# Performance work log

Hardware: AMD Instinct MI355X
Metric: run time of the kernel (lower is better)

## Reference

```python
import jax, jax.numpy as jnp
import numpy as np

N_HEADS = 12
NEG_BIG = 1e10  # matches torch source's -10000000000.0 masking constant


def setup_inputs() -> dict:
    key = jax.random.key(0)
    ks = jax.random.split(key, 5)
    nb, ns, nf = 4, 2048, 768
    return {
        "x": jax.random.normal(ks[0], (nb, ns, nf), dtype=jnp.float32),
        "Wqkv_w": jax.random.normal(ks[1], (3 * nf, nf), dtype=jnp.float32) * 0.02,
        "Wqkv_b": jax.random.normal(ks[2], (3 * nf,), dtype=jnp.float32) * 0.02,
        "Wproj_w": jax.random.normal(ks[3], (nf, nf), dtype=jnp.float32) * 0.02,
        "Wproj_b": jax.random.normal(ks[4], (nf,), dtype=jnp.float32) * 0.02,
    }


def reference(x, Wqkv_w, Wqkv_b, Wproj_w, Wproj_b):
    nb, ns, nf = x.shape
    hd = nf // N_HEADS
    qkv = x @ Wqkv_w.T + Wqkv_b            # [b, s, 3f]
    q = qkv[..., :nf]                       # source bug: k and v are taken from q
    q = q.reshape(nb, ns, N_HEADS, hd).transpose(0, 2, 1, 3)  # [b, h, s, d]
    k = q
    v = q
    w = jnp.einsum("bhqd,bhkd->bhqk", q, k) * (1.0 / jnp.sqrt(jnp.float32(hd)))
    mask = jnp.tril(jnp.ones((ns, ns), dtype=x.dtype))
    w = jax.nn.softmax(w * mask - NEG_BIG * (1.0 - mask), axis=-1)
    a = jnp.einsum("bhqk,bhkd->bhqd", w, v)
    a = a.transpose(0, 2, 1, 3).reshape(nb, ns, nf)
    return a @ Wproj_w.T + Wproj_b
```

## Files before the change

kernel.cpp:

```cpp
#include <hip/hip_runtime.h>
#include <hip/hip_bf16.h>

#define NF 768
#define NHEADS 12
#define NSEQ 2048
#define LDG 40

#define QSC 0.42466090f

typedef __attribute__((__ext_vector_type__(8))) __bf16 bfrag;
typedef __attribute__((__ext_vector_type__(4))) float f32x4;
typedef __attribute__((__ext_vector_type__(16))) float f32x16;

static __device__ __forceinline__ unsigned short bfu(float f) {
    union { __hip_bfloat16 h; unsigned short u; } v;
    v.h = __float2bfloat16(f);
    return v.u;
}

static __device__ __forceinline__ int packrn(float lo, float hi) {
    union { __hip_bfloat162 h; int i; } u;
    u.h.x = __float2bfloat16(lo);
    u.h.y = __float2bfloat16(hi);
    return u.i;
}

static __device__ __forceinline__ void cvt16(const float4* v, uint4* out2) {
    unsigned* o = (unsigned*)out2;
#pragma unroll
    for (int i = 0; i < 4; i++) {
        o[2*i]   = (unsigned)packrn(v[i].x, v[i].y);
        o[2*i+1] = (unsigned)packrn(v[i].z, v[i].w);
    }
}

static __device__ __forceinline__ float exp2a(float x) {
#if __has_builtin(__builtin_amdgcn_exp2f)
    return __builtin_amdgcn_exp2f(x);
#else
    return exp2f(x);
#endif
}

static __device__ __forceinline__ void plswap(int& a, int& b, int hi) {
#if __has_builtin(__builtin_amdgcn_permlane32_swap)
    auto r = __builtin_amdgcn_permlane32_swap((unsigned)a, (unsigned)b, false, false);
    a = (int)r[0]; b = (int)r[1];
#else
    int ta = __shfl_xor(b, 32), tb = __shfl_xor(a, 32);
    a = hi ? ta : a;
    b = hi ? b : tb;
#endif
}

static __device__ __forceinline__ float xhalf(float v, int hi) {
#if __has_builtin(__builtin_amdgcn_permlane32_swap)
    union { float f; unsigned u; } c; c.f = v;
    auto r = __builtin_amdgcn_permlane32_swap(c.u, c.u, false, false);
    union { unsigned u; float f; } d; d.u = hi ? r[0] : r[1];
    return d.f;
#else
    return __shfl_xor(v, 32);
#endif
}

__global__ __launch_bounds__(256) void gemm_qkv(const float* __restrict__ x,
                                                const float* __restrict__ W,
                                                const float* __restrict__ bias,
                                                unsigned short* __restrict__ Qo) {
    __shared__ unsigned short As[64][LDG];
    __shared__ unsigned short Bs[128][LDG];
    const int t    = threadIdx.x;
    const int bm   = blockIdx.x / 6, bn = blockIdx.x % 6;
    const int m0   = bm * 64, n0 = bn * 128;
    const int lane = t & 63;
    const int wid  = t >> 6;
    const int wm   = (wid >> 1) * 32, wn = (wid & 1) * 64;

    const int arow = t >> 2, acol = (t & 3) * 8;
    const int brow = t >> 1, bcol = (t & 1) * 16;
    const float* ag = x + (size_t)(m0 + arow) * NF + acol;
    const float* bg = W + (size_t)(n0 + brow) * NF + bcol;

    f32x4 acc[2][4];
#pragma unroll
    for (int i = 0; i < 2; i++)
#pragma unroll
        for (int j = 0; j < 4; j++) acc[i][j] = (f32x4)0.0f;

    for (int k0 = 0; k0 < NF; k0 += 32) {
        float4 a0 = *(const float4*)(ag + k0);
        float4 a1 = *(const float4*)(ag + k0 + 4);
        float4 bv[4];
#pragma unroll
        for (int i = 0; i < 4; i++) bv[i] = *(const float4*)(bg + k0 + i*4);
        uint4 pa;
        pa.x = (unsigned)packrn(a0.x, a0.y);
        pa.y = (unsigned)packrn(a0.z, a0.w);
        pa.z = (unsigned)packrn(a1.x, a1.y);
        pa.w = (unsigned)packrn(a1.z, a1.w);
        uint4 pb[2];
        cvt16(bv, pb);
        *(uint4*)&As[arow][acol]    = pa;
        *(uint4*)&Bs[brow][bcol]     = pb[0];
        *(uint4*)&Bs[brow][bcol + 8] = pb[1];
        __syncthreads();

        bfrag af[2], bfr[4];
#pragma unroll
        for (int i = 0; i < 2; i++)
            af[i]  = *(const bfrag*)&As[wm + i*16 + (lane & 15)][(lane >> 4) * 8];
#pragma unroll
        for (int j = 0; j < 4; j++)
            bfr[j] = *(const bfrag*)&Bs[wn + j*16 + (lane & 15)][(lane >> 4) * 8];
#pragma unroll
        for (int i = 0; i < 2; i++)
#pragma unroll
            for (int j = 0; j < 4; j++)
                acc[i][j] = __builtin_amdgcn_mfma_f32_16x16x32_bf16(af[i], bfr[j], acc[i][j], 0, 0, 0);
        __syncthreads();
    }

#pragma unroll
    for (int j = 0; j < 4; j++) {
        const int col = n0 + wn + j*16 + (lane & 15);
        const float bvv = bias[col];
#pragma unroll
        for (int i = 0; i < 2; i++) {
            const int rbase = m0 + wm + i*16 + ((lane >> 4) << 2);
#pragma unroll
            for (int r = 0; r < 4; r++)
                Qo[(size_t)(rbase + r) * NF + col] = bfu((acc[i][j][r] + bvv) * QSC);
        }
    }
}

__global__ __launch_bounds__(256) void gemm_proj(const unsigned short* __restrict__ A,
                                                 const float* __restrict__ W,
                                                 const float* __restrict__ bias,
                                                 float* __restrict__ out) {
    __shared__ unsigned short As[64][LDG];
    __shared__ unsigned short Bs[128][LDG];
    const int t    = threadIdx.x;
    const int bm   = blockIdx.x / 6, bn = blockIdx.x % 6;
    const int m0   = bm * 64, n0 = bn * 128;
    const int lane = t & 63;
    const int wid  = t >> 6;
    const int wm   = (wid >> 1) * 32, wn = (wid & 1) * 64;

    const int arow = t >> 2, acol = (t & 3) * 8;
    const int brow = t >> 1, bcol = (t & 1) * 16;
    const unsigned short* ag = A + (size_t)(m0 + arow) * NF + acol;
    const float*          bg = W + (size_t)(n0 + brow) * NF + bcol;

    f32x4 acc[2][4];
#pragma unroll
    for (int i = 0; i < 2; i++)
#pragma unroll
        for (int j = 0; j < 4; j++) acc[i][j] = (f32x4)0.0f;

    for (int k0 = 0; k0 < NF; k0 += 32) {
        uint4 va = *(const uint4*)(ag + k0);
        float4 bv[4];
#pragma unroll
        for (int i = 0; i < 4; i++) bv[i] = *(const float4*)(bg + k0 + i*4);
        uint4 pb[2];
        cvt16(bv, pb);
        *(uint4*)&As[arow][acol]     = va;
        *(uint4*)&Bs[brow][bcol]     = pb[0];
        *(uint4*)&Bs[brow][bcol + 8] = pb[1];
        __syncthreads();

        bfrag af[2], bfr[4];
#pragma unroll
        for (int i = 0; i < 2; i++)
            af[i]  = *(const bfrag*)&As[wm + i*16 + (lane & 15)][(lane >> 4) * 8];
#pragma unroll
        for (int j = 0; j < 4; j++)
            bfr[j] = *(const bfrag*)&Bs[wn + j*16 + (lane & 15)][(lane >> 4) * 8];
#pragma unroll
        for (int i = 0; i < 2; i++)
#pragma unroll
            for (int j = 0; j < 4; j++)
                acc[i][j] = __builtin_amdgcn_mfma_f32_16x16x32_bf16(af[i], bfr[j], acc[i][j], 0, 0, 0);
        __syncthreads();
    }

#pragma unroll
    for (int j = 0; j < 4; j++) {
        const int col = n0 + wn + j*16 + (lane & 15);
        const float bvv = bias[col];
#pragma unroll
        for (int i = 0; i < 2; i++) {
            const int rbase = m0 + wm + i*16 + ((lane >> 4) << 2);
#pragma unroll
            for (int r = 0; r < 4; r++)
                out[(size_t)(rbase + r) * NF + col] = acc[i][j][r] + bvv;
        }
    }
}

__global__ __launch_bounds__(128, 1) void attn(const unsigned short* __restrict__ Q,
                                               unsigned short* __restrict__ O) {
    const int pair = blockIdx.x;
    const int bh   = blockIdx.y;
    const int b    = bh / NHEADS, h = bh % NHEADS;
    const unsigned short* base = Q + (size_t)b * NSEQ * NF + h * 64;
    unsigned short*       ob   = O + (size_t)b * NSEQ * NF + h * 64;

    const int t   = threadIdx.x;
    const int w   = t >> 6;
    const int l31 = t & 31;
    const int hi  = (t >> 5) & 1;
    const int sw  = l31 & 7;
    const int svw = (l31 & 7) ^ ((l31 >> 2) & 7);

    __shared__ unsigned short Ks[64 * 64];
    __shared__ unsigned short Vt[64 * 64];

    for (int half = 0; half < 2; half++) {
        const int qt  = half ? (31 - pair) : pair;
        const int wq0 = qt * 64 + w * 32;
        const int qg  = wq0 + l31;

        bfrag qf[4];
#pragma unroll
        for (int c16 = 0; c16 < 4; c16++)
            qf[c16] = *(const bfrag*)(base + (size_t)qg * NF + c16*16 + hi*8);

        f32x16 o[2];
#pragma unroll
        for (int fd = 0; fd < 2; fd++)
#pragma unroll
            for (int r = 0; r < 16; r++) o[fd][r] = 0.0f;
        float m_ = -3.0e38f, l_ = 0.0f;

        const int ktend = qt + 1;
        for (int kt = 0; kt < ktend; kt++) {
            const int k0 = kt * 64;

            {
                const int r = t >> 1, c = t & 1;
                const unsigned short* kg = base + (size_t)(k0 + r) * NF + c * 32;
#pragma unroll
                for (int i = 0; i < 4; i++) {
                    uint4 v = *(const uint4*)(kg + i * 8);
                    const int u = (4 * c + i) ^ (r & 7);
                    *(uint4*)&Ks[r * 64 + u * 8] = v;
                }
            }
            {
                const int p = t & 15, g2 = t >> 4;
                const unsigned short* vg = base + (size_t)(k0 + 8 * g2) * NF + 4 * p;
                uint2 ld[8];
#pragma unroll
                for (int i = 0; i < 8; i++) ld[i] = *(const uint2*)(vg + (size_t)i * NF);
#pragma unroll
                for (int j = 0; j < 4; j++) {
                    const int d = 4 * p + j;
                    union { unsigned short h[8]; uint4 q; } wv;
#pragma unroll
                    for (int i = 0; i < 8; i++) wv.h[i] = ((const unsigned short*)&ld[i])[j];
                    const int u = g2 ^ (d & 7) ^ ((d >> 2) & 7);
                    *(uint4*)&Vt[d * 64 + u * 8] = wv.q;
                }
            }
            __syncthreads();

            const bool diag  = (kt == qt);
            const int  kb_hi = diag ? w : 1;

            f32x16 s[2];
            __builtin_amdgcn_s_setprio(1);
#pragma unroll
            for (int kblk = 0; kblk < 2; kblk++) {
                if (kblk <= kb_hi) {
                    f32x16 z;
#pragma unroll
                    for (int r = 0; r < 16; r++) z[r] = 0.0f;
#pragma unroll
                    for (int c16 = 0; c16 < 4; c16++) {
                        bfrag ka = *(const bfrag*)&Ks[(kblk*32 + l31)*64 + (((2*c16 + hi) ^ sw) * 8)];
                        z = __builtin_amdgcn_mfma_f32_32x32x16_bf16(ka, qf[c16], z, 0, 0, 0);
                    }
                    s[kblk] = z;
                }
            }
            __builtin_amdgcn_s_setprio(0);

            if (diag) {
                if (w == 0) {
#pragma unroll
                    for (int r = 0; r < 16; r++) {
                        const int kp = k0 + (r & 3) + 8*(r >> 2) + 4*hi;
                        if (kp > qg) s[0][r] = -1.0e30f;
                    }
                } else {
#pragma unroll
                    for (int r = 0; r < 16; r++) {
                        const int kp = k0 + 32 + (r & 3) + 8*(r >> 2) + 4*hi;
                        if (kp > qg) s[1][r] = -1.0e30f;
                    }
                }
            }

            float mx = -3.0e38f;
#pragma unroll
            for (int kblk = 0; kblk < 2; kblk++)
                if (kblk <= kb_hi) {
#pragma unroll
                    for (int r = 0; r < 16; r++) mx = fmaxf(mx, s[kblk][r]);
                }
            mx = fmaxf(mx, xhalf(mx, hi));

            const bool nogrow = __all(mx <= m_);
            const float mn = nogrow ? m_ : fmaxf(m_, mx);
            float rs = 0.0f;
#pragma unroll
            for (int kblk = 0; kblk < 2; kblk++)
                if (kblk <= kb_hi) {
#pragma unroll
                    for (int r = 0; r < 16; r++) {
                        const float p = exp2a(s[kblk][r] - mn);
                        s[kblk][r] = p;
                        rs += p;
                    }
                }
            rs += xhalf(rs, hi);
            if (nogrow) {
                l_ += rs;
            } else {
                const float sc = exp2a(m_ - mn);
                l_ = l_ * sc + rs;
                m_ = mn;
#pragma unroll
                for (int fd = 0; fd < 2; fd++)
#pragma unroll
                    for (int r = 0; r < 16; r++) o[fd][r] *= sc;
            }

#pragma unroll
            for (int kblk = 0; kblk < 2; kblk++) {
                if (kblk <= kb_hi) {
                    int wv_[4][2];
#pragma unroll
                    for (int f = 0; f < 4; f++)
#pragma unroll
                        for (int rr = 0; rr < 2; rr++)
                            wv_[f][rr] = packrn(s[kblk][4*f + 2*rr], s[kblk][4*f + 2*rr + 1]);
#pragma unroll
                    for (int c = 0; c < 2; c++) {
                        int x0 = wv_[2*c][0], y0 = wv_[2*c+1][0];
                        plswap(x0, y0, hi);
                        int x1 = wv_[2*c][1], y1 = wv_[2*c+1][1];
                        plswap(x1, y1, hi);
                        union { int d[4]; bfrag f; } pf;
                        pf.d[0] = x0; pf.d[1] = x1; pf.d[2] = y0; pf.d[3] = y1;
                        const int ck = kblk*2 + c;
                        __builtin_amdgcn_s_setprio(1);
#pragma unroll
                        for (int fd = 0; fd < 2; fd++) {
                            bfrag va = *(const bfrag*)&Vt[(fd*32 + l31)*64 + (((2*ck + hi) ^ svw) * 8)];
                            o[fd] = __builtin_amdgcn_mfma_f32_32x32x16_bf16(va, pf.f, o[fd], 0, 0, 0);
                        }
                        __builtin_amdgcn_s_setprio(0);
                    }
                }
            }
            __syncthreads();
        }

        const float inv = 1.0f / (l_ * QSC);
#pragma unroll
        for (int fd = 0; fd < 2; fd++)
#pragma unroll
            for (int f = 0; f < 4; f++) {
                const int d0 = fd*32 + 8*f + 4*hi;
                uint2 pr;
                pr.x = (unsigned)packrn(o[fd][4*f+0]*inv, o[fd][4*f+1]*inv);
                pr.y = (unsigned)packrn(o[fd][4*f+2]*inv, o[fd][4*f+3]*inv);
                *(uint2*)(ob + (size_t)qg * NF + d0) = pr;
            }
    }
}

extern "C" void kernel_launch(void* const* d_in, const int* in_sizes, int n_in,
                              void* d_out, int out_size, void* d_ws, size_t ws_size,
                              hipStream_t stream) {
    const float* x    = (const float*)d_in[0];
    const float* Wqkv = (const float*)d_in[1];
    const float* bqkv = (const float*)d_in[2];
    const float* Wp   = (const float*)d_in[3];
    const float* bp   = (const float*)d_in[4];
    float* out        = (float*)d_out;

    unsigned short* Qws = (unsigned short*)d_ws;
    unsigned short* Aws = Qws + (size_t)8192 * NF;

    gemm_qkv<<<768, 256, 0, stream>>>(x, Wqkv, bqkv, Qws);
    attn<<<dim3(16, 48), 128, 0, stream>>>(Qws, Aws);
    gemm_proj<<<768, 256, 0, stream>>>(Aws, Wp, bp, out);
}
```

Baseline: 144.3 us.

## Pre-convert inputs to bf16 and stream GEMM tiles with direct global-to-LDS loads

```diff
diff --git a/kernel.cpp b/kernel.cpp
--- a/kernel.cpp
+++ b/kernel.cpp
@@ -4,7 +4,8 @@
 #define NF 768
 #define NHEADS 12
 #define NSEQ 2048
-#define LDG 40
+#define NX (8192 * 768)
+#define NW (768 * 768)
 
 #define QSC 0.42466090f
 
@@ -23,15 +24,6 @@
     u.h.x = __float2bfloat16(lo);
     u.h.y = __float2bfloat16(hi);
     return u.i;
-}
-
-static __device__ __forceinline__ void cvt16(const float4* v, uint4* out2) {
-    unsigned* o = (unsigned*)out2;
-#pragma unroll
-    for (int i = 0; i < 4; i++) {
-        o[2*i]   = (unsigned)packrn(v[i].x, v[i].y);
-        o[2*i+1] = (unsigned)packrn(v[i].z, v[i].w);
-    }
 }
 
 static __device__ __forceinline__ float exp2a(float x) {
@@ -64,12 +56,51 @@
 #endif
 }
 
-__global__ __launch_bounds__(256) void gemm_qkv(const float* __restrict__ x,
-                                                const float* __restrict__ W,
+static __device__ __forceinline__ void gload16(const unsigned short* g, unsigned short* l) {
+#if __has_builtin(__builtin_amdgcn_global_load_lds)
+    __builtin_amdgcn_global_load_lds(
+        (const __attribute__((address_space(1))) void*)g,
+        (__attribute__((address_space(3))) void*)l, 16, 0, 0);
+#else
+    *(uint4*)l = *(const uint4*)g;
+#endif
+}
+
+__global__ __launch_bounds__(256) void preconv(const float* __restrict__ x,
+                                               const float* __restrict__ W1,
+                                               const float* __restrict__ W2,
+                                               unsigned short* __restrict__ xb,
+                                               unsigned short* __restrict__ W1b,
+                                               unsigned short* __restrict__ W2b) {
+    const size_t i = ((size_t)blockIdx.x * 256 + threadIdx.x) * 8;
+    const float* src;
+    unsigned short* dst;
+    float scl = 1.0f;
+    if (i < (size_t)NX) {
+        src = x + i; dst = xb + i;
+    } else if (i < (size_t)NX + NW) {
+        const size_t j = i - NX;
+        src = W1 + j; dst = W1b + j; scl = QSC;
+    } else {
+        const size_t j = i - NX - NW;
+        src = W2 + j; dst = W2b + j;
+    }
+    float4 v0 = *(const float4*)(src);
+    float4 v1 = *(const float4*)(src + 4);
+    uint4 o;
+    o.x = (unsigned)packrn(v0.x * scl, v0.y * scl);
+    o.y = (unsigned)packrn(v0.z * scl, v0.w * scl);
+    o.z = (unsigned)packrn(v1.x * scl, v1.y * scl);
+    o.w = (unsigned)packrn(v1.z * scl, v1.w * scl);
+    *(uint4*)dst = o;
+}
+
+__global__ __launch_bounds__(256) void gemm_qkv(const unsigned short* __restrict__ A,
+                                                const unsigned short* __restrict__ B,
                                                 const float* __restrict__ bias,
                                                 unsigned short* __restrict__ Qo) {
-    __shared__ unsigned short As[64][LDG];
-    __shared__ unsigned short Bs[128][LDG];
+    __shared__ unsigned short As[64 * 32];
+    __shared__ unsigned short Bs[128 * 32];
     const int t    = threadIdx.x;
     const int bm   = blockIdx.x / 6, bn = blockIdx.x % 6;
     const int m0   = bm * 64, n0 = bn * 128;
@@ -77,10 +108,9 @@
     const int wid  = t >> 6;
     const int wm   = (wid >> 1) * 32, wn = (wid & 1) * 64;
 
-    const int arow = t >> 2, acol = (t & 3) * 8;
-    const int brow = t >> 1, bcol = (t & 1) * 16;
-    const float* ag = x + (size_t)(m0 + arow) * NF + acol;
-    const float* bg = W + (size_t)(n0 + brow) * NF + bcol;
+    const unsigned short* ga  = A + (size_t)(m0 + (t >> 2)) * NF + (t & 3) * 8;
+    const unsigned short* gb  = B + (size_t)(n0 + (t >> 2)) * NF + (t & 3) * 8;
+    const unsigned short* gb2 = gb + (size_t)64 * NF;
 
     f32x4 acc[2][4];
 #pragma unroll
@@ -89,30 +119,18 @@
         for (int j = 0; j < 4; j++) acc[i][j] = (f32x4)0.0f;
 
     for (int k0 = 0; k0 < NF; k0 += 32) {
-        float4 a0 = *(const float4*)(ag + k0);
-        float4 a1 = *(const float4*)(ag + k0 + 4);
-        float4 bv[4];
-#pragma unroll
-        for (int i = 0; i < 4; i++) bv[i] = *(const float4*)(bg + k0 + i*4);
-        uint4 pa;
-        pa.x = (unsigned)packrn(a0.x, a0.y);
-        pa.y = (unsigned)packrn(a0.z, a0.w);
-        pa.z = (unsigned)packrn(a1.x, a1.y);
-        pa.w = (unsigned)packrn(a1.z, a1.w);
-        uint4 pb[2];
-        cvt16(bv, pb);
-        *(uint4*)&As[arow][acol]    = pa;
-        *(uint4*)&Bs[brow][bcol]     = pb[0];
-        *(uint4*)&Bs[brow][bcol + 8] = pb[1];
+        gload16(ga + k0, &As[t * 8]);
+        gload16(gb + k0, &Bs[t * 8]);
+        gload16(gb2 + k0, &Bs[2048 + t * 8]);
         __syncthreads();
 
         bfrag af[2], bfr[4];
 #pragma unroll
         for (int i = 0; i < 2; i++)
-            af[i]  = *(const bfrag*)&As[wm + i*16 + (lane & 15)][(lane >> 4) * 8];
+            af[i]  = *(const bfrag*)&As[(wm + i*16 + (lane & 15)) * 32 + (lane >> 4) * 8];
 #pragma unroll
         for (int j = 0; j < 4; j++)
-            bfr[j] = *(const bfrag*)&Bs[wn + j*16 + (lane & 15)][(lane >> 4) * 8];
+            bfr[j] = *(const bfrag*)&Bs[(wn + j*16 + (lane & 15)) * 32 + (lane >> 4) * 8];
 #pragma unroll
         for (int i = 0; i < 2; i++)
 #pragma unroll
@@ -124,23 +142,23 @@
 #pragma unroll
     for (int j = 0; j < 4; j++) {
         const int col = n0 + wn + j*16 + (lane & 15);
-        const float bvv = bias[col];
+        const float bq = QSC * bias[col];
 #pragma unroll
         for (int i = 0; i < 2; i++) {
             const int rbase = m0 + wm + i*16 + ((lane >> 4) << 2);
 #pragma unroll
             for (int r = 0; r < 4; r++)
-                Qo[(size_t)(rbase + r) * NF + col] = bfu((acc[i][j][r] + bvv) * QSC);
+                Qo[(size_t)(rbase + r) * NF + col] = bfu(acc[i][j][r] + bq);
         }
     }
 }
 
 __global__ __launch_bounds__(256) void gemm_proj(const unsigned short* __restrict__ A,
-                                                 const float* __restrict__ W,
+                                                 const unsigned short* __restrict__ B,
                                                  const float* __restrict__ bias,
                                                  float* __restrict__ out) {
-    __shared__ unsigned short As[64][LDG];
-    __shared__ unsigned short Bs[128][LDG];
+    __shared__ unsigned short As[64 * 32];
+    __shared__ unsigned short Bs[128 * 32];
     const int t    = threadIdx.x;
     const int bm   = blockIdx.x / 6, bn = blockIdx.x % 6;
     const int m0   = bm * 64, n0 = bn * 128;
@@ -148,10 +166,9 @@
     const int wid  = t >> 6;
     const int wm   = (wid >> 1) * 32, wn = (wid & 1) * 64;
 
-    const int arow = t >> 2, acol = (t & 3) * 8;
-    const int brow = t >> 1, bcol = (t & 1) * 16;
-    const unsigned short* ag = A + (size_t)(m0 + arow) * NF + acol;
-    const float*          bg = W + (size_t)(n0 + brow) * NF + bcol;
+    const unsigned short* ga  = A + (size_t)(m0 + (t >> 2)) * NF + (t & 3) * 8;
+    const unsigned short* gb  = B + (size_t)(n0 + (t >> 2)) * NF + (t & 3) * 8;
+    const unsigned short* gb2 = gb + (size_t)64 * NF;
 
     f32x4 acc[2][4];
 #pragma unroll
@@ -160,24 +177,18 @@
         for (int j = 0; j < 4; j++) acc[i][j] = (f32x4)0.0f;
 
     for (int k0 = 0; k0 < NF; k0 += 32) {
-        uint4 va = *(const uint4*)(ag + k0);
-        float4 bv[4];
-#pragma unroll
-        for (int i = 0; i < 4; i++) bv[i] = *(const float4*)(bg + k0 + i*4);
-        uint4 pb[2];
-        cvt16(bv, pb);
-        *(uint4*)&As[arow][acol]     = va;
-        *(uint4*)&Bs[brow][bcol]     = pb[0];
-        *(uint4*)&Bs[brow][bcol + 8] = pb[1];
+        gload16(ga + k0, &As[t * 8]);
+        gload16(gb + k0, &Bs[t * 8]);
+        gload16(gb2 + k0, &Bs[2048 + t * 8]);
         __syncthreads();
 
         bfrag af[2], bfr[4];
 #pragma unroll
         for (int i = 0; i < 2; i++)
-            af[i]  = *(const bfrag*)&As[wm + i*16 + (lane & 15)][(lane >> 4) * 8];
+            af[i]  = *(const bfrag*)&As[(wm + i*16 + (lane & 15)) * 32 + (lane >> 4) * 8];
 #pragma unroll
         for (int j = 0; j < 4; j++)
-            bfr[j] = *(const bfrag*)&Bs[wn + j*16 + (lane & 15)][(lane >> 4) * 8];
+            bfr[j] = *(const bfrag*)&Bs[(wn + j*16 + (lane & 15)) * 32 + (lane >> 4) * 8];
 #pragma unroll
         for (int i = 0; i < 2; i++)
 #pragma unroll
@@ -313,7 +324,7 @@
                 }
             mx = fmaxf(mx, xhalf(mx, hi));
 
-            const bool nogrow = __all(mx <= m_);
+            const bool nogrow = __all(mx <= m_ + 8.0f);
             const float mn = nogrow ? m_ : fmaxf(m_, mx);
             float rs = 0.0f;
 #pragma unroll
@@ -395,9 +406,13 @@
     float* out        = (float*)d_out;
 
     unsigned short* Qws = (unsigned short*)d_ws;
-    unsigned short* Aws = Qws + (size_t)8192 * NF;
-
-    gemm_qkv<<<768, 256, 0, stream>>>(x, Wqkv, bqkv, Qws);
+    unsigned short* Aws = Qws + (size_t)NX;
+    unsigned short* xb  = Aws + (size_t)NX;
+    unsigned short* W1b = xb + (size_t)NX;
+    unsigned short* W2b = W1b + (size_t)NW;
+
+    preconv<<<3648, 256, 0, stream>>>(x, Wqkv, Wp, xb, W1b, W2b);
+    gemm_qkv<<<768, 256, 0, stream>>>(xb, W1b, bqkv, Qws);
     attn<<<dim3(16, 48), 128, 0, stream>>>(Qws, Aws);
-    gemm_proj<<<768, 256, 0, stream>>>(Aws, Wp, bp, out);
-}
+    gemm_proj<<<768, 256, 0, stream>>>(Aws, W2b, bp, out);
+}
```

Result: faster. 131.6 us (-8.8%).
